# Optimization experiments

Hardware: AMD Instinct MI355X
Metric: run time of the kernel (lower is better)

## Reference

```python
import jax, jax.numpy as jnp
import numpy as np

B, L, C, H, FF = 2, 2048, 1024, 16, 4096
HD = C // H
SCALE = HD ** -0.5
EPS = 1e-5


def _ln(x, g, b):
    m = jnp.mean(x, axis=-1, keepdims=True)
    v = jnp.mean((x - m) ** 2, axis=-1, keepdims=True)
    return (x - m) * jax.lax.rsqrt(v + EPS) * g + b


def setup_inputs() -> dict:
    key = jax.random.key(0)
    ks = jax.random.split(key, 12)
    s = lambda fan_in: 1.0 / np.sqrt(fan_in)
    return {
        "x": jax.random.normal(ks[0], (B, L, C), jnp.float32),
        "freq_diff": jax.random.normal(ks[1], (B, L), jnp.float32),
        "qkv_w": jax.random.normal(ks[2], (C, 3 * C), jnp.float32) * s(C),
        "qkv_b": jnp.zeros((3 * C,), jnp.float32),
        "fp_w1": jax.random.normal(ks[3], (1, C), jnp.float32),
        "fp_b1": jnp.zeros((C,), jnp.float32),
        "fp_ln_g": jnp.ones((C,), jnp.float32),
        "fp_ln_b": jnp.zeros((C,), jnp.float32),
        "fp_w2": jax.random.normal(ks[4], (C, C), jnp.float32) * s(C),
        "fp_b2": jnp.zeros((C,), jnp.float32),
        "wq_w": jax.random.normal(ks[5], (HD, HD), jnp.float32) * s(HD),
        "wq_b": jnp.zeros((HD,), jnp.float32),
        "wk_w": jax.random.normal(ks[6], (HD, HD), jnp.float32) * s(HD),
        "wk_b": jnp.zeros((HD,), jnp.float32),
        "out_w": jax.random.normal(ks[7], (C, C), jnp.float32) * s(C),
        "out_b": jnp.zeros((C,), jnp.float32),
        "n1_g": jnp.ones((C,), jnp.float32),
        "n1_b": jnp.zeros((C,), jnp.float32),
        "n2_g": jnp.ones((C,), jnp.float32),
        "n2_b": jnp.zeros((C,), jnp.float32),
        "mlp_w1": jax.random.normal(ks[8], (C, FF), jnp.float32) * s(C),
        "mlp_b1": jnp.zeros((FF,), jnp.float32),
        "mlp_w2": jax.random.normal(ks[9], (FF, C), jnp.float32) * s(FF),
        "mlp_b2": jnp.zeros((C,), jnp.float32),
        "freq_scale": jnp.ones((1,), jnp.float32),
    }


def reference(x, freq_diff, qkv_w, qkv_b, fp_w1, fp_b1, fp_ln_g, fp_ln_b,
              fp_w2, fp_b2, wq_w, wq_b, wk_w, wk_b, out_w, out_b,
              n1_g, n1_b, n2_g, n2_b, mlp_w1, mlp_b1, mlp_w2, mlp_b2,
              freq_scale):
    shortcut = x
    xn = _ln(x, n1_g, n1_b)
    qkv = (xn @ qkv_w + qkv_b).reshape(B, L, 3, H, HD)
    qkv = jnp.transpose(qkv, (2, 0, 3, 1, 4))  # [3,B,H,L,HD]
    q, k, v = qkv[0], qkv[1], qkv[2]

    # frequency bias: MLP on scalar freq_diff -> per-head bias vectors
    fb = freq_diff[..., None] @ fp_w1 + fp_b1          # [B,L,C]
    fb = jax.nn.gelu(_ln(fb, fp_ln_g, fp_ln_b), approximate=False)
    fb = fb @ fp_w2 + fp_b2                            # [B,L,C]
    fb = jnp.transpose(fb.reshape(B, L, H, HD), (0, 2, 1, 3))  # [B,H,L,HD]
    qb = fb @ wq_w + wq_b
    kb = fb @ wk_w + wk_b
    freq_attn_bias = jnp.einsum('bhqd,bhkd->bhqk', qb, kb)

    attn = jnp.einsum('bhqd,bhkd->bhqk', q, k) * SCALE
    attn = attn + freq_scale[0] * freq_attn_bias
    attn = jax.nn.softmax(attn, axis=-1)
    o = jnp.einsum('bhqk,bhkd->bhqd', attn, v)
    o = jnp.transpose(o, (0, 2, 1, 3)).reshape(B, L, C)
    x = shortcut + (o @ out_w + out_b)

    xn2 = _ln(x, n2_g, n2_b)
    h = jax.nn.gelu(xn2 @ mlp_w1 + mlp_b1, approximate=False)
    x = x + (h @ mlp_w2 + mlp_b2)
    return x
```

## Files before the change

kernel.cpp:

```cpp
#include <hip/hip_runtime.h>
#include <math.h>


typedef __bf16 bf16;
typedef float f32x4 __attribute__((ext_vector_type(4)));
typedef bf16 bf16x8 __attribute__((ext_vector_type(8)));
typedef bf16 bf16x4 __attribute__((ext_vector_type(4)));

#define DEVINL __device__ __forceinline__

#define LOG2E 1.4426950408889634f

DEVINL float fast_exp2(float x) { return __builtin_amdgcn_exp2f(x); }

DEVINL void async_load16(const void* g, void* l) {
  __builtin_amdgcn_global_load_lds(
      (const __attribute__((address_space(1))) unsigned int*)g,
      (__attribute__((address_space(3))) unsigned int*)l, 16, 0, 0);
}

DEVINL f32x4 mfma16(bf16x8 a, bf16x8 b, f32x4 c) {
  return __builtin_amdgcn_mfma_f32_16x16x32_bf16(a, b, c, 0, 0, 0);
}

DEVINL float gelu_exact(float v) {
  return 0.5f * v * (1.0f + erff(v * 0.70710678118654752f));
}

DEVINL void hard_barrier() {
  asm volatile("" ::: "memory");
  __builtin_amdgcn_s_barrier();
  asm volatile("" ::: "memory");
}

DEVINL void block_reduce2(float& a, float& b, float* red, int tid) {
#pragma unroll
  for (int off = 32; off >= 1; off >>= 1) {
    a += __shfl_xor(a, off);
    b += __shfl_xor(b, off);
  }
  int w = tid >> 6;
  if ((tid & 63) == 0) { red[2 * w] = a; red[2 * w + 1] = b; }
  __syncthreads();
  a = red[0] + red[2] + red[4] + red[6];
  b = red[1] + red[3] + red[5] + red[7];
  __syncthreads();
}

__global__ __launch_bounds__(256) void pre_kernel(
    const float* __restrict__ fp_w2, const float* __restrict__ fp_b2,
    const float* __restrict__ wq_w, const float* __restrict__ wq_b,
    const float* __restrict__ wk_w, const float* __restrict__ wk_b,
    bf16* __restrict__ wqk2t, float* __restrict__ bqk,
    const float* __restrict__ qkv_w, const float* __restrict__ out_w,
    const float* __restrict__ mlp_w1, const float* __restrict__ mlp_w2,
    bf16* __restrict__ qkv_wt, bf16* __restrict__ out_wt,
    bf16* __restrict__ w1t, bf16* __restrict__ w2t,
    const float* __restrict__ x, const float* __restrict__ fd,
    const float* __restrict__ g1, const float* __restrict__ b1,
    const float* __restrict__ fw1, const float* __restrict__ fb1,
    const float* __restrict__ flg, const float* __restrict__ flb,
    bf16* __restrict__ xn, bf16* __restrict__ gout) {
  __shared__ __align__(16) char smem[49152];
  const int id = blockIdx.x, t = threadIdx.x;

  if (id < 256) {
    float* Wl = (float*)smem;
    float* Al = (float*)(smem + 16384);
    const int sel = id >> 7, h = (id >> 3) & 15, ck = id & 7;
    const float* wsel = sel ? wk_w : wq_w;
#pragma unroll
    for (int i = 0; i < 4; ++i)
      ((float4*)Wl)[i * 256 + t] = ((const float4*)wsel)[i * 256 + t];
    const int c0 = ck * 128, off = h * 64;
#pragma unroll
    for (int it = 0; it < 8; ++it) {
      int idx = it * 256 + t;
      int rr = idx >> 4, c4 = idx & 15;
      float4 v = *(const float4*)(fp_w2 + (size_t)(c0 + rr) * 1024 + off + c4 * 4);
      float vv[4] = {v.x, v.y, v.z, v.w};
#pragma unroll
      for (int k = 0; k < 4; ++k) {
        int i2 = c4 * 4 + k;
        Al[i2 * 128 + (rr ^ (i2 & 31))] = vv[k];
      }
    }
    __syncthreads();
    const int cr = t & 127, jh = (t >> 7) * 32;
    float acc[32];
#pragma unroll
    for (int j = 0; j < 32; ++j) acc[j] = 0.f;
    for (int i = 0; i < 64; ++i) {
      float a = Al[i * 128 + (cr ^ (i & 31))];
      const float4* wrow = (const float4*)(Wl + i * 64 + jh);
#pragma unroll
      for (int j4 = 0; j4 < 8; ++j4) {
        float4 wv = wrow[j4];
        acc[j4 * 4 + 0] += a * wv.x;
        acc[j4 * 4 + 1] += a * wv.y;
        acc[j4 * 4 + 2] += a * wv.z;
        acc[j4 * 4 + 3] += a * wv.w;
      }
    }
    const int nbase = sel * 1024 + off + jh;
#pragma unroll
    for (int j = 0; j < 32; ++j)
      wqk2t[(size_t)(nbase + j) * 1024 + c0 + cr] = (bf16)acc[j];
    if (ck == 0 && t < 64) {
      float s = 0.f;
      for (int i = 0; i < 64; ++i) s += fp_b2[off + i] * Wl[i * 64 + t];
      bqk[sel * 1024 + off + t] = s + (sel ? wk_b[t] : wq_b[t]);
    }
    return;
  }

  if (id < 12544) {
    float (*tile)[33] = (float(*)[33])smem;
    int i0 = id - 256;
    const float* W; bf16* Wt; int K, N, bx, by;
    if (i0 < 3072) {
      W = qkv_w; Wt = qkv_wt; K = 1024; N = 3072; bx = i0 % 96; by = i0 / 96;
    } else if (i0 < 4096) {
      int i = i0 - 3072;
      W = out_w; Wt = out_wt; K = 1024; N = 1024; bx = i & 31; by = i >> 5;
    } else if (i0 < 8192) {
      int i = i0 - 4096;
      W = mlp_w1; Wt = w1t; K = 1024; N = 4096; bx = i & 127; by = i >> 7;
    } else {
      int i = i0 - 8192;
      W = mlp_w2; Wt = w2t; K = 4096; N = 1024; bx = i & 31; by = i >> 5;
    }
    int n0 = bx * 32, k0 = by * 32;
    int tx = t & 31, ty = t >> 5;
#pragma unroll
    for (int r = 0; r < 4; ++r)
      tile[ty + r * 8][tx] = W[(size_t)(k0 + ty + r * 8) * N + n0 + tx];
    __syncthreads();
#pragma unroll
    for (int r = 0; r < 4; ++r)
      Wt[(size_t)(n0 + ty + r * 8) * K + k0 + tx] = (bf16)tile[tx][ty + r * 8];
    return;
  }

  float* red = (float*)smem;
  int tok = id - 12544;
  float4 xv = ((const float4*)(x + (size_t)tok * 1024))[t];
  float s = xv.x + xv.y + xv.z + xv.w;
  float ss = xv.x * xv.x + xv.y * xv.y + xv.z * xv.z + xv.w * xv.w;
  block_reduce2(s, ss, red, t);
  float mean = s * (1.0f / 1024.0f);
  float rsig = rsqrtf(ss * (1.0f / 1024.0f) - mean * mean + 1e-5f);
  float4 g4 = ((const float4*)g1)[t], b4 = ((const float4*)b1)[t];
  bf16x4 o;
  o[0] = (bf16)((xv.x - mean) * rsig * g4.x + b4.x);
  o[1] = (bf16)((xv.y - mean) * rsig * g4.y + b4.y);
  o[2] = (bf16)((xv.z - mean) * rsig * g4.z + b4.z);
  o[3] = (bf16)((xv.w - mean) * rsig * g4.w + b4.w);
  ((bf16x4*)xn)[(size_t)tok * 256 + t] = o;

  float dv = fd[tok];
  float4 w4 = ((const float4*)fw1)[t], c4 = ((const float4*)fb1)[t];
  float f0 = dv * w4.x + c4.x, f1 = dv * w4.y + c4.y;
  float f2 = dv * w4.z + c4.z, f3 = dv * w4.w + c4.w;
  s = f0 + f1 + f2 + f3;
  ss = f0 * f0 + f1 * f1 + f2 * f2 + f3 * f3;
  block_reduce2(s, ss, red, t);
  mean = s * (1.0f / 1024.0f);
  rsig = rsqrtf(ss * (1.0f / 1024.0f) - mean * mean + 1e-5f);
  float4 lg = ((const float4*)flg)[t], lb = ((const float4*)flb)[t];
  bf16x4 q;
  q[0] = (bf16)gelu_exact((f0 - mean) * rsig * lg.x + lb.x);
  q[1] = (bf16)gelu_exact((f1 - mean) * rsig * lg.y + lb.y);
  q[2] = (bf16)gelu_exact((f2 - mean) * rsig * lg.z + lb.z);
  q[3] = (bf16)gelu_exact((f3 - mean) * rsig * lg.w + lb.w);
  ((bf16x4*)gout)[(size_t)tok * 256 + t] = q;
}

__global__ __launch_bounds__(256) void reduce_oln(
    const float* __restrict__ part, const float* __restrict__ x,
    const float* __restrict__ outb, const float* __restrict__ b2,
    const float* __restrict__ g, const float* __restrict__ bb,
    float* __restrict__ out0, bf16* __restrict__ ln2) {
  __shared__ float red[8];
  int tok = blockIdx.x, t = threadIdx.x;
  size_t base = (size_t)tok * 256 + t;
  const size_t S = (size_t)4096 * 256;
  float4 p0 = ((const float4*)part)[base];
  float4 p1 = ((const float4*)part)[base + S];
  float4 xv = ((const float4*)x)[base];
  float4 ob = ((const float4*)outb)[t];
  float v0 = xv.x + p0.x + p1.x + ob.x;
  float v1 = xv.y + p0.y + p1.y + ob.y;
  float v2 = xv.z + p0.z + p1.z + ob.z;
  float v3 = xv.w + p0.w + p1.w + ob.w;
  float s = v0 + v1 + v2 + v3;
  float ss = v0 * v0 + v1 * v1 + v2 * v2 + v3 * v3;
  block_reduce2(s, ss, red, t);
  float mean = s * (1.0f / 1024.0f);
  float rsig = rsqrtf(ss * (1.0f / 1024.0f) - mean * mean + 1e-5f);
  float4 g4 = ((const float4*)g)[t], bb4 = ((const float4*)bb)[t];
  bf16x4 o;
  o[0] = (bf16)((v0 - mean) * rsig * g4.x + bb4.x);
  o[1] = (bf16)((v1 - mean) * rsig * g4.y + bb4.y);
  o[2] = (bf16)((v2 - mean) * rsig * g4.z + bb4.z);
  o[3] = (bf16)((v3 - mean) * rsig * g4.w + bb4.w);
  ((bf16x4*)ln2)[base] = o;
  float4 b24 = ((const float4*)b2)[t];
  float4 ov;
  ov.x = v0 + b24.x; ov.y = v1 + b24.y; ov.z = v2 + b24.z; ov.w = v3 + b24.w;
  ((float4*)out0)[base] = ov;
}

#define PHASE_LOADS(MH, NH, LA, LB, BFR)                                      \
    if (LA) {                                                                 \
      _Pragma("unroll") for (int ml = 0; ml < 4; ++ml) {                      \
        _Pragma("unroll") for (int ks = 0; ks < 2; ++ks) {                    \
          const int rr = ml * 16 + lm;                                        \
          const int cc = (((ks * 4 + quad) ^ (lm & 7)) << 3);                 \
          af[ml][ks] = *(const bf16x8*)&As[bsel][MH][wm][rr][cc];             \
        }                                                                     \
      }                                                                       \
    }                                                                         \
    if (LB) {                                                                 \
      _Pragma("unroll") for (int nl = 0; nl < 2; ++nl) {                      \
        _Pragma("unroll") for (int ks = 0; ks < 2; ++ks) {                    \
          const int rr = nl * 16 + lm;                                        \
          const int cc = (((ks * 4 + quad) ^ (lm & 7)) << 3);                 \
          BFR[nl][ks] = *(const bf16x8*)&Bs[bsel][NH][wn][rr][cc];            \
        }                                                                     \
      }                                                                       \
    }

#define PHASE_MFMA(MH, NH, BFR)                                               \
    _Pragma("unroll") for (int ks = 0; ks < 2; ++ks) {                        \
      _Pragma("unroll") for (int ml = 0; ml < 4; ++ml) {                      \
        _Pragma("unroll") for (int nl = 0; nl < 2; ++nl) {                    \
          acc[(MH)*4 + ml][(NH)*2 + nl] = mfma16(                             \
              af[ml][ks], BFR[nl][ks], acc[(MH)*4 + ml][(NH)*2 + nl]);        \
        }                                                                     \
      }                                                                       \
    }

#define PHASE(MH, NH, LA, LB, BFR, STAGE_STMT, WAIT_STMT)                     \
  do {                                                                        \
    PHASE_LOADS(MH, NH, LA, LB, BFR)                                          \
    STAGE_STMT;                                                               \
    WAIT_STMT;                                                                \
    hard_barrier();                                                           \
    __builtin_amdgcn_s_setprio(1);                                            \
    PHASE_MFMA(MH, NH, BFR)                                                   \
    __builtin_amdgcn_s_setprio(0);                                            \
  } while (0)

template <class Epi>
__global__ __launch_bounds__(512, 2) void gemm256(
    const bf16* __restrict__ A, const bf16* __restrict__ Bt,
    int lda, int ldb, int K, int kstride, int nbx, int nblk, int rowoffz,
    Epi epi) {
  __shared__ __align__(16) bf16 As[2][2][2][64][64];
  __shared__ __align__(16) bf16 Bs[2][2][4][32][64];

  const int tid = threadIdx.x;
  const int lane = tid & 63, w = tid >> 6;
  const int quad = lane >> 4, lm = lane & 15;
  const int wm = w >> 2, wn = w & 3;

  const int kz = blockIdx.x / nblk;
  const int bid = blockIdx.x - kz * nblk;
  const int swz = (nblk & 7) ? bid : ((bid & 7) * (nblk >> 3) + (bid >> 3));
  const int tm = swz / nbx, tn = swz - tm * nbx;
  const int m0 = tm << 8, n0 = tn << 8;
  const int rowoff = kz * rowoffz;
  A += (size_t)kz * kstride;
  Bt += (size_t)kz * kstride;

  const bf16* Abase = A + (size_t)m0 * lda;
  const bf16* Bbase = Bt + (size_t)n0 * ldb;

  auto stageA = [&](int b, int mh, int kt) {
#pragma unroll
    for (int j = 0; j < 2; ++j) {
      const int q = (w * 2 + j) * 64 + lane;
      const int wm2 = q >> 9, rr = (q >> 3) & 63, c = q & 7;
      async_load16(Abase + (size_t)(wm2 * 128 + mh * 64 + rr) * lda +
                       (size_t)kt * 64 + ((c ^ (rr & 7)) << 3),
                   (char*)&As[b][mh][0][0][0] + (w * 2 + j) * 1024);
    }
  };
  auto stageB = [&](int b, int nh, int kt) {
#pragma unroll
    for (int j = 0; j < 2; ++j) {
      const int q = (w * 2 + j) * 64 + lane;
      const int wn4 = q >> 8, rr = (q >> 3) & 31, c = q & 7;
      async_load16(Bbase + (size_t)(wn4 * 64 + nh * 32 + rr) * ldb +
                       (size_t)kt * 64 + ((c ^ (rr & 7)) << 3),
                   (char*)&Bs[b][nh][0][0][0] + (w * 2 + j) * 1024);
    }
  };

  f32x4 acc[8][4];
#pragma unroll
  for (int i = 0; i < 8; ++i)
#pragma unroll
    for (int j = 0; j < 4; ++j) {
      acc[i][j][0] = 0.f; acc[i][j][1] = 0.f;
      acc[i][j][2] = 0.f; acc[i][j][3] = 0.f;
    }
  bf16x8 af[4][2], bfrA[2][2], bfrB[2][2];

  stageA(0, 0, 0);
  stageB(0, 1, 0);
  stageA(0, 1, 0);
  stageB(0, 0, 0);
  stageA(1, 0, 1);
  stageB(1, 1, 1);
  asm volatile("s_waitcnt vmcnt(4)" ::: "memory");
  hard_barrier();

  const int nt = K >> 6;
  int bsel = 0;
  for (int t = 0; t < nt; ++t, bsel ^= 1) {
    PHASE(0, 0, 1, 1, bfrA, { if (t + 1 < nt) stageA(bsel ^ 1, 1, t + 1); }, {});
    PHASE(0, 1, 0, 1, bfrB, { if (t + 1 < nt) stageB(bsel ^ 1, 0, t + 1); }, {});
    PHASE(1, 1, 1, 0, bfrB, { if (t + 2 < nt) stageA(bsel, 0, t + 2); }, {});
    PHASE(1, 0, 0, 0, bfrA, { if (t + 2 < nt) stageB(bsel, 1, t + 2); },
          {
            if (t + 2 < nt) {
              asm volatile("s_waitcnt vmcnt(4)" ::: "memory");
            } else if (t + 1 < nt) {
              asm volatile("s_waitcnt vmcnt(0)" ::: "memory");
            }
          });
  }

#pragma unroll
  for (int mi = 0; mi < 8; ++mi)
#pragma unroll
    for (int ni = 0; ni < 4; ++ni)
      epi(rowoff + m0 + wm * 128 + mi * 16 + quad * 4,
          n0 + wn * 64 + ni * 16 + lm, acc[mi][ni]);
}

__global__ __launch_bounds__(256) void reduce_mlp2(
    const float* __restrict__ part, float* __restrict__ out) {
  size_t i = (size_t)blockIdx.x * 256 + threadIdx.x;
  const float4* p = (const float4*)part;
  float4 o = ((const float4*)out)[i];
  const size_t S = (size_t)4096 * 256;
  float4 a = p[i], b = p[i + S], c = p[i + 2 * S], d = p[i + 3 * S];
  o.x += a.x + b.x + c.x + d.x;
  o.y += a.y + b.y + c.y + d.y;
  o.z += a.z + b.z + c.z + d.z;
  o.w += a.w + b.w + c.w + d.w;
  ((float4*)out)[i] = o;
}

struct EpiQKV {
  const float* __restrict__ bias;
  bf16 *Qc, *Kc, *Vt;
  DEVINL void operator()(int row, int col, f32x4 v) const {
    int b = row >> 11, l = row & 2047;
    float bia = bias[col];
    if (col < 1024) {
      int h = col >> 6, d = col & 63;
      bf16* p = Qc + (size_t)(((b << 4) + h) * 2048 + l) * 128 + d;
#pragma unroll
      for (int r = 0; r < 4; ++r) p[r * 128] = (bf16)((v[r] + bia) * (0.125f * LOG2E));
    } else if (col < 2048) {
      int c2 = col - 1024, h = c2 >> 6, d = c2 & 63;
      bf16* p = Kc + (size_t)(((b << 4) + h) * 2048 + l) * 128 + d;
#pragma unroll
      for (int r = 0; r < 4; ++r) p[r * 128] = (bf16)(v[r] + bia);
    } else {
      int c2 = col - 2048, h = c2 >> 6, d = c2 & 63;
      bf16x4 pk;
#pragma unroll
      for (int r = 0; r < 4; ++r) pk[r] = (bf16)(v[r] + bia);
      *(bf16x4*)(Vt + (size_t)(((b << 4) + h) * 64 + d) * 2048 + l) = pk;
    }
  }
};

struct EpiQBKB {
  const float* __restrict__ bias;
  const float* __restrict__ fs;
  bf16 *Qc, *Kc;
  DEVINL void operator()(int row, int col, f32x4 v) const {
    int b = row >> 11, l = row & 2047;
    float bia = bias[col];
    if (col < 1024) {
      int h = col >> 6, d = col & 63;
      float sc = fs[0] * LOG2E;
      bf16* p = Qc + (size_t)(((b << 4) + h) * 2048 + l) * 128 + 64 + d;
#pragma unroll
      for (int r = 0; r < 4; ++r) p[r * 128] = (bf16)((v[r] + bia) * sc);
    } else {
      int c2 = col - 1024, h = c2 >> 6, d = c2 & 63;
      bf16* p = Kc + (size_t)(((b << 4) + h) * 2048 + l) * 128 + 64 + d;
#pragma unroll
      for (int r = 0; r < 4; ++r) p[r * 128] = (bf16)(v[r] + bia);
    }
  }
};

struct EpiMLP1 {
  const float* __restrict__ bias;
  bf16* hbf;
  DEVINL void operator()(int row, int col, f32x4 v) const {
    float bia = bias[col];
#pragma unroll
    for (int r = 0; r < 4; ++r)
      hbf[(size_t)(row + r) * 4096 + col] = (bf16)gelu_exact(v[r] + bia);
  }
};

struct EpiPart {
  float* part;
  DEVINL void operator()(int row, int col, f32x4 v) const {
#pragma unroll
    for (int r = 0; r < 4; ++r)
      part[(size_t)(row + r) * 1024 + col] = v[r];
  }
};

#define PSS 64

__global__ __launch_bounds__(512, 2) void flash_kernel(
    const bf16* __restrict__ Qc, const bf16* __restrict__ Kcp,
    const bf16* __restrict__ Vt, bf16* __restrict__ Obf) {
  __shared__ bf16 KsA[64 * 128];
  __shared__ bf16 KsB[64 * 128];
  __shared__ bf16 VsA[64 * 64];
  __shared__ bf16 VsB[64 * 64];
  __shared__ bf16 Ps[256 * PSS];

  const int tid = threadIdx.x, lane = tid & 63, w = tid >> 6;
  const int quad = lane >> 4, lm = lane & 15;
  const int id = blockIdx.x;
  const int bh = id & 31, qt = id >> 5;
  const int b = bh >> 4, h = bh & 15;
  const int qrw = w * 32;

  const bf16* Kg0 = Kcp + (size_t)bh * 2048 * 128;
  const bf16* Vg0 = Vt + (size_t)bh * 64 * 2048;

  auto stage = [&](int kv, bf16* Kdst, bf16* Vdst) {
    const bf16* Kg = Kg0 + (size_t)kv * 64 * 128;
#pragma unroll
    for (int i = 0; i < 2; ++i) {
      int ch = i * 512 + tid, key = ch >> 4, c = (ch & 15) ^ (key & 7);
      async_load16(Kg + (size_t)key * 128 + c * 8,
                   (char*)Kdst + (i * 512 + w * 64) * 16);
    }
    {
      int d = tid >> 3, c = (tid & 7) ^ (d & 7);
      async_load16(Vg0 + (size_t)d * 2048 + kv * 64 + c * 8,
                   (char*)Vdst + (w * 64) * 16);
    }
  };

  stage(0, KsA, VsA);

  const bf16* Qg = Qc + ((size_t)bh * 2048 + qt * 256) * 128;
  bf16x8 qf[2][4];
#pragma unroll
  for (int qh = 0; qh < 2; ++qh)
#pragma unroll
    for (int ks = 0; ks < 4; ++ks)
      qf[qh][ks] = *(const bf16x8*)(Qg + (size_t)(qrw + qh * 16 + lm) * 128 +
                                    (ks * 4 + quad) * 8);

  float m_run[2] = {-3.0e38f, -3.0e38f};
  float l_lane[2] = {0.f, 0.f};
  f32x4 o_acc[2][4];
#pragma unroll
  for (int qh = 0; qh < 2; ++qh)
#pragma unroll
    for (int nf = 0; nf < 4; ++nf) {
      o_acc[qh][nf][0] = 0.f; o_acc[qh][nf][1] = 0.f;
      o_acc[qh][nf][2] = 0.f; o_acc[qh][nf][3] = 0.f;
    }

  for (int kv = 0; kv < 32; ++kv) {
    const bf16* Kcur = (kv & 1) ? KsB : KsA;
    const bf16* Vcur = (kv & 1) ? VsB : VsA;
    __syncthreads();
    if (kv + 1 < 32)
      stage(kv + 1, (kv & 1) ? KsA : KsB, (kv & 1) ? VsA : VsB);

    f32x4 sa[2][4];
#pragma unroll
    for (int qh = 0; qh < 2; ++qh)
#pragma unroll
      for (int nk = 0; nk < 4; ++nk) {
        sa[qh][nk][0] = 0.f; sa[qh][nk][1] = 0.f;
        sa[qh][nk][2] = 0.f; sa[qh][nk][3] = 0.f;
      }
    __builtin_amdgcn_s_setprio(1);
#pragma unroll
    for (int ks = 0; ks < 4; ++ks) {
      bf16x8 ak[4];
#pragma unroll
      for (int nk = 0; nk < 4; ++nk) {
        int key = nk * 16 + lm;
        int pos = (ks * 4 + quad) ^ (key & 7);
        ak[nk] = *(const bf16x8*)(Kcur + key * 128 + pos * 8);
      }
#pragma unroll
      for (int nk = 0; nk < 4; ++nk) {
        sa[0][nk] = mfma16(ak[nk], qf[0][ks], sa[0][nk]);
        sa[1][nk] = mfma16(ak[nk], qf[1][ks], sa[1][nk]);
      }
    }
    __builtin_amdgcn_s_setprio(0);

#pragma unroll
    for (int qh = 0; qh < 2; ++qh) {
      float mx = fmaxf(fmaxf(sa[qh][0][0], sa[qh][0][1]), sa[qh][0][2]);
      mx = fmaxf(fmaxf(mx, sa[qh][0][3]), sa[qh][1][0]);
      mx = fmaxf(fmaxf(mx, sa[qh][1][1]), sa[qh][1][2]);
      mx = fmaxf(fmaxf(mx, sa[qh][1][3]), sa[qh][2][0]);
      mx = fmaxf(fmaxf(mx, sa[qh][2][1]), sa[qh][2][2]);
      mx = fmaxf(fmaxf(mx, sa[qh][2][3]), sa[qh][3][0]);
      mx = fmaxf(fmaxf(mx, sa[qh][3][1]), sa[qh][3][2]);
      mx = fmaxf(mx, sa[qh][3][3]);
      mx = fmaxf(mx, __shfl_xor(mx, 16));
      mx = fmaxf(mx, __shfl_xor(mx, 32));
      if (__any(mx > m_run[qh] + 8.0f)) {
        float mnew = fmaxf(m_run[qh], mx);
        float alpha = fast_exp2(m_run[qh] - mnew);
        m_run[qh] = mnew;
        l_lane[qh] *= alpha;
#pragma unroll
        for (int nf = 0; nf < 4; ++nf) {
          o_acc[qh][nf][0] *= alpha; o_acc[qh][nf][1] *= alpha;
          o_acc[qh][nf][2] *= alpha; o_acc[qh][nf][3] *= alpha;
        }
      }
      float rs = 0.f;
#pragma unroll
      for (int nk = 0; nk < 4; ++nk)
#pragma unroll
        for (int rg = 0; rg < 4; ++rg) {
          float pv = fast_exp2(sa[qh][nk][rg] - m_run[qh]);
          sa[qh][nk][rg] = pv;
          rs += pv;
        }
      l_lane[qh] += rs;

      int qr = qrw + qh * 16 + lm;
#pragma unroll
      for (int nk = 0; nk < 4; ++nk) {
        int c16 = 2 * nk + (quad >> 1);
        int cs = c16 ^ (lm & 7);
        bf16x4 pk;
        pk[0] = (bf16)sa[qh][nk][0]; pk[1] = (bf16)sa[qh][nk][1];
        pk[2] = (bf16)sa[qh][nk][2]; pk[3] = (bf16)sa[qh][nk][3];
        *(bf16x4*)(Ps + qr * PSS + cs * 8 + (quad & 1) * 4) = pk;
      }
    }

#pragma unroll
    for (int ks = 0; ks < 2; ++ks) {
      bf16x8 vb[4], pa[2];
#pragma unroll
      for (int nf = 0; nf < 4; ++nf) {
        int d = nf * 16 + lm;
        int cs = (ks * 4 + quad) ^ (d & 7);
        vb[nf] = *(const bf16x8*)(Vcur + d * 64 + cs * 8);
      }
#pragma unroll
      for (int qh = 0; qh < 2; ++qh) {
        int qr = qrw + qh * 16 + lm;
        int cs = (ks * 4 + quad) ^ (lm & 7);
        pa[qh] = *(const bf16x8*)(Ps + qr * PSS + cs * 8);
      }
      __builtin_amdgcn_s_setprio(1);
#pragma unroll
      for (int qh = 0; qh < 2; ++qh)
#pragma unroll
        for (int nf = 0; nf < 4; ++nf)
          o_acc[qh][nf] = mfma16(vb[nf], pa[qh], o_acc[qh][nf]);
      __builtin_amdgcn_s_setprio(0);
    }
  }

#pragma unroll
  for (int qh = 0; qh < 2; ++qh) {
    float lt = l_lane[qh];
    lt += __shfl_xor(lt, 16);
    lt += __shfl_xor(lt, 32);
    float inv = 1.0f / lt;
    int l = qt * 256 + qrw + qh * 16 + lm;
#pragma unroll
    for (int nf = 0; nf < 4; ++nf) {
      bf16x4 ov;
#pragma unroll
      for (int rg = 0; rg < 4; ++rg) ov[rg] = (bf16)(o_acc[qh][nf][rg] * inv);
      int d = h * 64 + nf * 16 + quad * 4;
      *(bf16x4*)(Obf + ((size_t)b * 2048 + l) * 1024 + d) = ov;
    }
  }
}

extern "C" void kernel_launch(void* const* d_in, const int* in_sizes, int n_in,
                              void* d_out, int out_size, void* d_ws, size_t ws_size,
                              hipStream_t stream) {
  (void)in_sizes; (void)n_in; (void)out_size; (void)ws_size;
  const float* x      = (const float*)d_in[0];
  const float* fd     = (const float*)d_in[1];
  const float* qkv_w  = (const float*)d_in[2];
  const float* qkv_b  = (const float*)d_in[3];
  const float* fp_w1  = (const float*)d_in[4];
  const float* fp_b1  = (const float*)d_in[5];
  const float* fp_ln_g= (const float*)d_in[6];
  const float* fp_ln_b= (const float*)d_in[7];
  const float* fp_w2  = (const float*)d_in[8];
  const float* fp_b2  = (const float*)d_in[9];
  const float* wq_w   = (const float*)d_in[10];
  const float* wq_b   = (const float*)d_in[11];
  const float* wk_w   = (const float*)d_in[12];
  const float* wk_b   = (const float*)d_in[13];
  const float* out_w  = (const float*)d_in[14];
  const float* out_b  = (const float*)d_in[15];
  const float* n1_g   = (const float*)d_in[16];
  const float* n1_b   = (const float*)d_in[17];
  const float* n2_g   = (const float*)d_in[18];
  const float* n2_b   = (const float*)d_in[19];
  const float* mlp_w1 = (const float*)d_in[20];
  const float* mlp_b1 = (const float*)d_in[21];
  const float* mlp_w2 = (const float*)d_in[22];
  const float* mlp_b2 = (const float*)d_in[23];
  const float* fscale = (const float*)d_in[24];
  float* out = (float*)d_out;

  char* p = (char*)d_ws;
  auto take = [&](size_t n) { char* r = p; p += (n + 255) & ~(size_t)255; return r; };
  bf16* xn_bf  = (bf16*)take((size_t)4096 * 1024 * 2);
  bf16* g_bf   = (bf16*)take((size_t)4096 * 1024 * 2);
  bf16* Qc     = (bf16*)take((size_t)32 * 2048 * 128 * 2);
  bf16* Kc     = (bf16*)take((size_t)32 * 2048 * 128 * 2);
  bf16* Vt     = (bf16*)take((size_t)32 * 64 * 2048 * 2);
  bf16* o_bf   = (bf16*)take((size_t)4096 * 1024 * 2);
  bf16* ln2_bf = (bf16*)take((size_t)4096 * 1024 * 2);
  bf16* h_bf   = (bf16*)take((size_t)4096 * 4096 * 2);
  bf16* qkv_wt = (bf16*)take((size_t)3072 * 1024 * 2);
  bf16* out_wt = (bf16*)take((size_t)1024 * 1024 * 2);
  bf16* w1t    = (bf16*)take((size_t)4096 * 1024 * 2);
  bf16* w2t    = (bf16*)take((size_t)1024 * 4096 * 2);
  bf16* wqk2t  = (bf16*)take((size_t)2048 * 1024 * 2);
  float* bqk   = (float*)take((size_t)2048 * 4);

  float* part = (float*)xn_bf;
  float* opart = (float*)h_bf;

  dim3 b256(256), b512(512);

  pre_kernel<<<dim3(16640), b256, 0, stream>>>(
      fp_w2, fp_b2, wq_w, wq_b, wk_w, wk_b, wqk2t, bqk,
      qkv_w, out_w, mlp_w1, mlp_w2, qkv_wt, out_wt, w1t, w2t,
      x, fd, n1_g, n1_b, fp_w1, fp_b1, fp_ln_g, fp_ln_b, xn_bf, g_bf);

  gemm256<<<dim3(192), b512, 0, stream>>>(xn_bf, qkv_wt, 1024, 1024, 1024, 0,
                                          12, 192, 0, EpiQKV{qkv_b, Qc, Kc, Vt});
  gemm256<<<dim3(128), b512, 0, stream>>>(g_bf, wqk2t, 1024, 1024, 1024, 0,
                                          8, 128, 0, EpiQBKB{bqk, fscale, Qc, Kc});
  flash_kernel<<<dim3(256), dim3(512), 0, stream>>>(Qc, Kc, Vt, o_bf);

  gemm256<<<dim3(128), b512, 0, stream>>>(o_bf, out_wt, 1024, 1024, 512, 512,
                                          4, 64, 4096, EpiPart{opart});
  reduce_oln<<<dim3(4096), b256, 0, stream>>>(opart, x, out_b, mlp_b2,
                                              n2_g, n2_b, out, ln2_bf);
  gemm256<<<dim3(256), b512, 0, stream>>>(ln2_bf, w1t, 1024, 1024, 1024, 0,
                                          16, 256, 0, EpiMLP1{mlp_b1, h_bf});
  gemm256<<<dim3(256), b512, 0, stream>>>(h_bf, w2t, 4096, 4096, 1024, 1024,
                                          4, 64, 4096, EpiPart{part});
  reduce_mlp2<<<dim3(4096), b256, 0, stream>>>(part, out);
}
```

Measured before the change: 450.4 us.

## Split flash attention over two KV halves with separate combine kernel

The flash attention kernel now splits the 2048-key range into two halves, launching 512 blocks instead of 256. Each block writes unnormalized fp32 partial outputs plus its running max and sum to workspace. A new combine kernel merges the two halves with log-sum-exp rescaling and writes bf16 output. The aim is to fill more CUs on a device with more CUs than 256 blocks can occupy, at the cost of extra global traffic for the fp32 partials and one more kernel launch.

New measurement: 466.1 us. 1.03x slower.

```diff
diff --git a/kernel.cpp b/kernel.cpp
--- a/kernel.cpp
+++ b/kernel.cpp
@@ -427,7 +427,8 @@
 
 __global__ __launch_bounds__(512, 2) void flash_kernel(
     const bf16* __restrict__ Qc, const bf16* __restrict__ Kcp,
-    const bf16* __restrict__ Vt, bf16* __restrict__ Obf) {
+    const bf16* __restrict__ Vt, float* __restrict__ Fpart,
+    float* __restrict__ Fml) {
   __shared__ bf16 KsA[64 * 128];
   __shared__ bf16 KsB[64 * 128];
   __shared__ bf16 VsA[64 * 64];
@@ -437,8 +438,10 @@
   const int tid = threadIdx.x, lane = tid & 63, w = tid >> 6;
   const int quad = lane >> 4, lm = lane & 15;
   const int id = blockIdx.x;
-  const int bh = id & 31, qt = id >> 5;
-  const int b = bh >> 4, h = bh & 15;
+  const int kvh = id >> 8;
+  const int r5 = id & 255;
+  const int bh = r5 & 31, qt = r5 >> 5;
+  const int kv0 = kvh * 16;
   const int qrw = w * 32;
 
   const bf16* Kg0 = Kcp + (size_t)bh * 2048 * 128;
@@ -459,7 +462,7 @@
     }
   };
 
-  stage(0, KsA, VsA);
+  stage(kv0, KsA, VsA);
 
   const bf16* Qg = Qc + ((size_t)bh * 2048 + qt * 256) * 128;
   bf16x8 qf[2][4];
@@ -481,11 +484,11 @@
       o_acc[qh][nf][2] = 0.f; o_acc[qh][nf][3] = 0.f;
     }
 
-  for (int kv = 0; kv < 32; ++kv) {
+  for (int kv = kv0; kv < kv0 + 16; ++kv) {
     const bf16* Kcur = (kv & 1) ? KsB : KsA;
     const bf16* Vcur = (kv & 1) ? VsB : VsA;
     __syncthreads();
-    if (kv + 1 < 32)
+    if (kv + 1 < kv0 + 16)
       stage(kv + 1, (kv & 1) ? KsA : KsB, (kv & 1) ? VsA : VsB);
 
     f32x4 sa[2][4];
@@ -585,22 +588,51 @@
     }
   }
 
+  const size_t rowbase = (size_t)(kvh * 32 + bh) * 2048;
 #pragma unroll
   for (int qh = 0; qh < 2; ++qh) {
     float lt = l_lane[qh];
     lt += __shfl_xor(lt, 16);
     lt += __shfl_xor(lt, 32);
-    float inv = 1.0f / lt;
     int l = qt * 256 + qrw + qh * 16 + lm;
+    float* Fp = Fpart + (rowbase + l) * 64;
 #pragma unroll
     for (int nf = 0; nf < 4; ++nf) {
-      bf16x4 ov;
-#pragma unroll
-      for (int rg = 0; rg < 4; ++rg) ov[rg] = (bf16)(o_acc[qh][nf][rg] * inv);
-      int d = h * 64 + nf * 16 + quad * 4;
-      *(bf16x4*)(Obf + ((size_t)b * 2048 + l) * 1024 + d) = ov;
-    }
-  }
+      float4 ov;
+      ov.x = o_acc[qh][nf][0]; ov.y = o_acc[qh][nf][1];
+      ov.z = o_acc[qh][nf][2]; ov.w = o_acc[qh][nf][3];
+      *(float4*)(Fp + nf * 16 + quad * 4) = ov;
+    }
+    if (quad == 0) {
+      float2 ml;
+      ml.x = m_run[qh]; ml.y = lt;
+      *(float2*)(Fml + (rowbase + l) * 2) = ml;
+    }
+  }
+}
+
+__global__ __launch_bounds__(256) void flash_combine(
+    const float* __restrict__ Fpart, const float* __restrict__ Fml,
+    bf16* __restrict__ Obf) {
+  size_t i = (size_t)blockIdx.x * 256 + threadIdx.x;
+  int hd4 = (int)(i & 15);
+  size_t row = i >> 4;
+  int bh = (int)(row >> 11), l = (int)(row & 2047);
+  int b = bh >> 4, h = bh & 15;
+  const size_t S = (size_t)32 * 2048;
+  float2 ml0 = ((const float2*)Fml)[row];
+  float2 ml1 = ((const float2*)Fml)[row + S];
+  float mmax = fmaxf(ml0.x, ml1.x);
+  float w0 = fast_exp2(ml0.x - mmax), w1 = fast_exp2(ml1.x - mmax);
+  float inv = 1.0f / (ml0.y * w0 + ml1.y * w1);
+  float4 o0 = ((const float4*)(Fpart + row * 64))[hd4];
+  float4 o1 = ((const float4*)(Fpart + (row + S) * 64))[hd4];
+  bf16x4 ov;
+  ov[0] = (bf16)((o0.x * w0 + o1.x * w1) * inv);
+  ov[1] = (bf16)((o0.y * w0 + o1.y * w1) * inv);
+  ov[2] = (bf16)((o0.z * w0 + o1.z * w1) * inv);
+  ov[3] = (bf16)((o0.w * w0 + o1.w * w1) * inv);
+  *(bf16x4*)(Obf + ((size_t)b * 2048 + l) * 1024 + h * 64 + hd4 * 4) = ov;
 }
 
 extern "C" void kernel_launch(void* const* d_in, const int* in_sizes, int n_in,
@@ -650,8 +682,10 @@
   bf16* w2t    = (bf16*)take((size_t)1024 * 4096 * 2);
   bf16* wqk2t  = (bf16*)take((size_t)2048 * 1024 * 2);
   float* bqk   = (float*)take((size_t)2048 * 4);
+  float* fml   = (float*)take((size_t)2 * 32 * 2048 * 2 * 4);
 
   float* part = (float*)xn_bf;
+  float* fpart = (float*)h_bf;
   float* opart = (float*)h_bf;
 
   dim3 b256(256), b512(512);
@@ -665,7 +699,8 @@
                                           12, 192, 0, EpiQKV{qkv_b, Qc, Kc, Vt});
   gemm256<<<dim3(128), b512, 0, stream>>>(g_bf, wqk2t, 1024, 1024, 1024, 0,
                                           8, 128, 0, EpiQBKB{bqk, fscale, Qc, Kc});
-  flash_kernel<<<dim3(256), dim3(512), 0, stream>>>(Qc, Kc, Vt, o_bf);
+  flash_kernel<<<dim3(512), dim3(512), 0, stream>>>(Qc, Kc, Vt, fpart, fml);
+  flash_combine<<<dim3(4096), b256, 0, stream>>>(fpart, fml, o_bf);
 
   gemm256<<<dim3(128), b512, 0, stream>>>(o_bf, out_wt, 1024, 1024, 512, 512,
                                           4, 64, 4096, EpiPart{opart});
```
